# Optimization experiments

Hardware: AMD Instinct MI355X
Metric: run time of the kernel (lower is better)

Reference implementation:

```python
import jax, jax.numpy as jnp
import numpy as np

B, C, H, W = 2, 256, 64, 64
HEADS, SR = 8, 4
D = C // HEADS          # head dim = 32
N = H * W               # query length = 4096
EPS = 1e-5


def _conv(x, w, stride=1, pad=0, groups=1, b=None):
    out = jax.lax.conv_general_dilated(
        x, w, (stride, stride), [(pad, pad), (pad, pad)],
        dimension_numbers=('NCHW', 'OIHW', 'NCHW'),
        feature_group_count=groups)
    if b is not None:
        out = out + b[None, :, None, None]
    return out


def _bn(x, p):
    # p: [4, C] = (gamma, beta, running_mean, running_var), eval-mode BN
    g, b, m, v = p[0], p[1], p[2], p[3]
    s = g / jnp.sqrt(v + EPS)
    return (x - m[None, :, None, None]) * s[None, :, None, None] + b[None, :, None, None]


def setup_inputs() -> dict:
    key = jax.random.key(0)
    ks = iter(jax.random.split(key, 32))
    nrm = lambda shape, s=0.05: jax.random.normal(next(ks), shape, jnp.float32) * s
    def bnp():
        return jnp.stack([jnp.ones((C,), jnp.float32), jnp.zeros((C,), jnp.float32),
                          jax.random.normal(next(ks), (C,), jnp.float32) * 0.1,
                          jax.random.uniform(next(ks), (C,), jnp.float32) + 0.5])
    return dict(
        x=jax.random.normal(next(ks), (B, C, H, W), jnp.float32),
        relative_pos_enc=jax.random.normal(next(ks), (B, 2, 64, 64), jnp.float32),
        q_w=nrm((C, C, 1, 1)), q_b=jnp.zeros((C,), jnp.float32),
        kv_w=nrm((2 * C, C, 1, 1)), kv_b=jnp.zeros((2 * C,), jnp.float32),
        sr1_dw_w=nrm((C, 1, SR + 3, SR + 3)), sr1_bn1=bnp(),
        sr1_pw_w=nrm((C, 1, 1, 1), 0.5), sr1_bn2=bnp(),
        sr2_dw_w=nrm((C, 1, SR // 2 + 3, SR // 2 + 3)), sr2_bn1=bnp(),
        sr2_pw_w=nrm((C, 1, 1, 1), 0.5), sr2_bn2=bnp(),
        local_w=nrm((C, 1, 3, 3)), local_b=jnp.zeros((C,), jnp.float32),
    )


def reference(x, relative_pos_enc, q_w, q_b, kv_w, kv_b,
              sr1_dw_w, sr1_bn1, sr1_pw_w, sr1_bn2,
              sr2_dw_w, sr2_bn1, sr2_pw_w, sr2_bn2,
              local_w, local_b):
    scale = D ** -0.5
    # q: 1x1 conv -> [B, heads, N, D]; both branches use the FIRST half of heads
    q = _conv(x, q_w, b=q_b).reshape(B, HEADS, D, N).transpose(0, 1, 3, 2)
    qh = q[:, :HEADS // 2]

    def branch(dw_w, bn1, pw_w, bn2, stride, pad, rpe_slice):
        # SR path: depthwise conv + BN + ReLU, depthwise 1x1 + BN
        y = jax.nn.relu(_bn(_conv(x, dw_w, stride, pad, groups=C), bn1))
        y = _bn(_conv(y, pw_w, groups=C), bn2)
        # local 3x3 depthwise mixing with residual
        y = _conv(y, local_w, pad=1, groups=C, b=local_b) + y
        kv = _conv(y, kv_w, b=kv_b)                # [B, 2C, h', w']
        k, v = jnp.split(kv, 2, axis=1)
        L = 2 * y.shape[2] * y.shape[3]            # channel-fold doubles kv length
        k = k.reshape(B, HEADS // 2, D, L)
        v = v.reshape(B, HEADS // 2, D, L).transpose(0, 1, 3, 2)
        attn = jnp.einsum('bhnd,bhdl->bhnl', qh, k) * scale
        rpe = jax.image.resize(rpe_slice, (B, 1, N, L), method='bicubic')
        attn = jax.nn.softmax(attn + rpe, axis=-1)
        return jnp.einsum('bhnl,bhld->bhnd', attn, v)

    x1 = branch(sr1_dw_w, sr1_bn1, sr1_pw_w, sr1_bn2,
                SR, (SR + 3) // 2, relative_pos_enc[:, 0:1])
    x2 = branch(sr2_dw_w, sr2_bn1, sr2_pw_w, sr2_bn2,
                SR // 2, (SR // 2 + 3) // 2, relative_pos_enc[:, 1:2])
    out = jnp.concatenate([x1, x2], axis=-1)       # [B, heads//2, N, 2D]
    return out.reshape(B, C, H, W)
```

## Files before the change

### kernel.cpp

```cpp
#include <hip/hip_runtime.h>
#include <hip/hip_bf16.h>
#include <math.h>

#define NB 2
#define NC 256
#define HWIN 4096
#define NN 4096
#define ND 32
#define NHH 4
#define EPSV 1e-5f

typedef short short8 __attribute__((ext_vector_type(8)));
typedef float f32x4 __attribute__((ext_vector_type(4)));
typedef unsigned short u16;
typedef unsigned int u32;

#define OFF_T1   0
#define OFF_Y1   131072
#define OFF_T2   262144
#define OFF_Y2   786432
#define OFF_Q    1310720
#define OFF_KT1  1835008
#define OFF_VT1  1900544
#define OFF_KT2  1966080
#define OFF_VT2  2228224
#define OFF_RCT1 2490368
#define OFF_RCT2 2531328
#define OFF_WT   2695168
#define OFF_PO   2826240
#define OFF_PS   4923392
#define OFF_QWT  5054464

#define QSCALE 0.2550437314857726f
#define LOG2E  1.4426950408889634f

__device__ __forceinline__ u16 f2bf(float x) {
  unsigned u = __float_as_uint(x);
  u += 0x7fffu + ((u >> 16) & 1u);
  return (u16)(u >> 16);
}

__device__ __forceinline__ u32 pk_bf16(float a, float b) {
  __hip_bfloat162 h = __float22bfloat162_rn(make_float2(a, b));
  u32 r; __builtin_memcpy(&r, &h, 4);
  return r;
}

__device__ __forceinline__ float keysw(float t) {
  t = fabsf(t);
  float w;
  if (t < 1.f)       w = ((1.5f*t - 2.5f)*t)*t + 1.f;
  else if (t < 2.f)  w = ((-0.5f*t + 2.5f)*t - 4.f)*t + 2.f;
  else               w = 0.f;
  return w;
}

template<int KS, int STR, int PAD, int OH>
__device__ __forceinline__ void dwconv_body(int idx, const float* __restrict__ x,
    const float* __restrict__ dww, const float* __restrict__ bn1,
    const float* __restrict__ pww, const float* __restrict__ bn2,
    float* __restrict__ tout) {
  const int hw = OH*OH;
  int s = idx % hw; int c = (idx/hw) % NC; int b = idx/(hw*NC);
  int oy = s / OH, ox = s % OH;
  const float* xp = x + (b*NC + c)*HWIN;
  const float* wp = dww + c*KS*KS;
  float acc = 0.f;
  #pragma unroll
  for (int ky = 0; ky < KS; ++ky) {
    int iy = oy*STR - PAD + ky;
    if (iy < 0 || iy >= 64) continue;
    #pragma unroll
    for (int kx = 0; kx < KS; ++kx) {
      int ix = ox*STR - PAD + kx;
      if (ix < 0 || ix >= 64) continue;
      acc += xp[iy*64 + ix] * wp[ky*KS + kx];
    }
  }
  float s1 = bn1[c] * rsqrtf(bn1[3*NC + c] + EPSV);
  float z = (acc - bn1[2*NC + c])*s1 + bn1[NC + c];
  z = fmaxf(z, 0.f);
  float s2 = bn2[c] * rsqrtf(bn2[3*NC + c] + EPSV);
  z = z * (pww[c]*s2) + (bn2[NC + c] - bn2[2*NC + c]*s2);
  tout[idx] = z;
}

__device__ __forceinline__ void rpe_body(int idx, const float* __restrict__ rpe,
                                         u16* __restrict__ rcT, int L, int ch) {
  int r = idx & 63; int l = (idx >> 6) % L; int b = idx / (64*L);
  float f = ((float)l + 0.5f)*(64.f/(float)L) - 0.5f;
  int i0 = (int)floorf(f) - 1;
  const float* rp = rpe + ((b*2 + ch)*64 + r)*64;
  float v = 0.f, wsum = 0.f;
  #pragma unroll
  for (int j = 0; j < 4; ++j) {
    int i = i0 + j;
    if (i >= 0 && i < 64) {
      float w = keysw(f - (float)i);
      v += w * rp[i]; wsum += w;
    }
  }
  rcT[((size_t)(b*L + l))*80 + 4 + r] = f2bf(v / wsum);
}

__global__ void __launch_bounds__(256) prep_kernel(
    const float* __restrict__ x,
    const float* __restrict__ dw1, const float* __restrict__ bn11,
    const float* __restrict__ pw1, const float* __restrict__ bn12, float* __restrict__ t1,
    const float* __restrict__ dw2, const float* __restrict__ bn21,
    const float* __restrict__ pw2, const float* __restrict__ bn22, float* __restrict__ t2,
    const float* __restrict__ rpe, u16* __restrict__ rct1, u16* __restrict__ rct2,
    const float* __restrict__ kvw, float* __restrict__ wt,
    const float* __restrict__ qw, float* __restrict__ qwt) {
  int blk = blockIdx.x;
  int t = threadIdx.x;
  if (blk < 512) {
    dwconv_body<7,4,3,16>(blk*256 + t, x, dw1, bn11, pw1, bn12, t1);
  } else if (blk < 2560) {
    dwconv_body<5,2,2,32>((blk-512)*256 + t, x, dw2, bn21, pw2, bn22, t2);
  } else if (blk < 2816) {
    rpe_body((blk-2560)*256 + t, rpe, rct1, 512, 0);
  } else if (blk < 3840) {
    rpe_body((blk-2816)*256 + t, rpe, rct2, 2048, 1);
  } else if (blk < 3968) {
    int base = ((blk-3840)*256 + t)*4;
    float4 vv = *(const float4*)(kvw + base);
    int o = base >> 8, c = base & 255;
    wt[(c+0)*512 + o] = vv.x;
    wt[(c+1)*512 + o] = vv.y;
    wt[(c+2)*512 + o] = vv.z;
    wt[(c+3)*512 + o] = vv.w;
  } else {
    int base = ((blk-3968)*256 + t)*4;
    float4 vv = *(const float4*)(qw + base);
    int oc = base >> 8, c = base & 255;
    qwt[(c+0)*128 + oc] = vv.x;
    qwt[(c+1)*128 + oc] = vv.y;
    qwt[(c+2)*128 + oc] = vv.z;
    qwt[(c+3)*128 + oc] = vv.w;
  }
}

template<int OH>
__device__ __forceinline__ void local_body(int idx, const float* __restrict__ tin,
    const float* __restrict__ lw, const float* __restrict__ lb, float* __restrict__ yout) {
  const int hw = OH*OH;
  int s = idx % hw; int c = (idx/hw) % NC; int b = idx/(hw*NC);
  int oy = s/OH, ox = s%OH;
  const float* tp = tin + (b*NC + c)*hw;
  const float* wp = lw + c*9;
  float acc = lb[c];
  #pragma unroll
  for (int ky = 0; ky < 3; ++ky) {
    int iy = oy - 1 + ky;
    if (iy < 0 || iy >= OH) continue;
    #pragma unroll
    for (int kx = 0; kx < 3; ++kx) {
      int ix = ox - 1 + kx;
      if (ix < 0 || ix >= OH) continue;
      acc += tp[iy*OH + ix]*wp[ky*3 + kx];
    }
  }
  yout[idx] = acc + tp[s];
}

__global__ void __launch_bounds__(256) local_kernel(
    const float* __restrict__ t1, const float* __restrict__ t2,
    const float* __restrict__ lw, const float* __restrict__ lb,
    float* __restrict__ y1, float* __restrict__ y2) {
  int blk = blockIdx.x, t = threadIdx.x;
  if (blk < 512) local_body<16>(blk*256 + t, t1, lw, lb, y1);
  else           local_body<32>((blk-512)*256 + t, t2, lw, lb, y2);
}

__global__ void __launch_bounds__(256) kv_kernel(
    const float* __restrict__ y1, const float* __restrict__ y2,
    const float* __restrict__ wt, const float* __restrict__ kvb,
    u16* __restrict__ kt1, u16* __restrict__ vt1,
    u16* __restrict__ kt2, u16* __restrict__ vt2,
    const float* __restrict__ x, const float* __restrict__ qwt,
    const float* __restrict__ qb, u16* __restrict__ q) {
  __shared__ float sbuf[NC*16];
  int blk = blockIdx.x, t = threadIdx.x;
  if (blk < 640) {
    const float* y; u16 *kT, *vT; int hw, b, s0;
    if (blk < 128) { y = y1; kT = kt1; vT = vt1; hw = 256;  b = blk >> 6;  s0 = (blk & 63)*4; }
    else { int v = blk-128; y = y2; kT = kt2; vT = vt2; hw = 1024; b = v >> 8; s0 = (v & 255)*4; }
    #pragma unroll
    for (int j = 0; j < 4; ++j) {
      int idx = t + 256*j;
      int c = idx >> 2, i = idx & 3;
      sbuf[idx] = y[(b*NC + c)*hw + s0 + i];
    }
    __syncthreads();
    int L = 2*hw;
    for (int half = 0; half < 2; ++half) {
      int o = t + half*256;
      const float* wr = wt + o;
      float bias = kvb[o];
      float acc[4];
      #pragma unroll
      for (int i = 0; i < 4; ++i) acc[i] = bias;
      #pragma unroll 4
      for (int c = 0; c < NC; ++c) {
        float w = wr[c*512];
        #pragma unroll
        for (int i = 0; i < 4; ++i) acc[i] += w*sbuf[c*4 + i];
      }
      int oc = o & 255;
      int hh2 = oc >> 6, r = oc & 63, d = r >> 1, e = r & 1;
      if (half == 0) {
        u16* kp = kT + ((size_t)((b*NHH + hh2)*L + e*hw + s0))*ND + d;
        #pragma unroll
        for (int i = 0; i < 4; ++i) kp[i*ND] = f2bf(acc[i]);
      } else {
        u16* vp = vT + ((size_t)((b*NHH + hh2)*ND + d))*L + e*hw + s0;
        #pragma unroll
        for (int i = 0; i < 4; ++i) vp[i] = f2bf(acc[i]);
      }
    }
  } else {
    int blk2 = blk - 640;
    int b = blk2 >> 8;
    int n0 = (blk2 & 255) * 16;
    #pragma unroll
    for (int j = 0; j < 16; ++j) {
      int idx = t + 256*j;
      int c = idx >> 4, i = idx & 15;
      sbuf[idx] = x[(b*NC + c)*HWIN + n0 + i];
    }
    __syncthreads();
    int half = t >> 7, oc = t & 127;
    float bias = qb[oc];
    float acc[8];
    #pragma unroll
    for (int i = 0; i < 8; ++i) acc[i] = bias;
    #pragma unroll 4
    for (int c = 0; c < NC; ++c) {
      float w = qwt[c*128 + oc];
      #pragma unroll
      for (int i = 0; i < 8; ++i) acc[i] += w * sbuf[c*16 + half*8 + i];
    }
    int h = oc >> 5, d = oc & 31;
    u16* qp = q + (((size_t)(b*NHH + h))*NN + n0 + half*8)*ND + d;
    #pragma unroll
    for (int i = 0; i < 8; ++i) qp[i*ND] = f2bf(acc[i]*QSCALE);
  }
}

__global__ void __launch_bounds__(256) attn_kernel(
    const u16* __restrict__ qbf,
    const u16* __restrict__ kt1, const u16* __restrict__ vt1, const u16* __restrict__ rct1,
    const u16* __restrict__ kt2, const u16* __restrict__ vt2, const u16* __restrict__ rct2,
    u32* __restrict__ po32, float* __restrict__ ps,
    float* __restrict__ out) {
  __shared__ u16 kbuf[2][64*72];
  __shared__ u16 vbuf[2][32*72];
  __shared__ u32 pbuf_all[4][16*36];
  int u = blockIdx.x;
  int br, b, hh, rb, chunk;
  if (u < 512) { br = 0; b = u >> 8; hh = (u >> 6) & 3; rb = u & 63; chunk = 0; }
  else { int v = u - 512; br = 1; chunk = v & 3; rb = (v >> 2) & 63; hh = (v >> 8) & 3; b = v >> 10; }
  int L = br ? 2048 : 512;
  const u16* kT  = br ? kt2 : kt1;
  const u16* vT  = br ? vt2 : vt1;
  const u16* rcT = br ? rct2 : rct1;
  int l0base = chunk * 512;
  int tid = threadIdx.x;
  int w = tid >> 6, lane = tid & 63;
  int g = lane >> 4, lo = lane & 15;
  u32* pbuf = pbuf_all[w];
  u16* pbuf16 = (u16*)pbuf;
  int n = rb*64 + w*16 + lo;

  const u16* kbase = kT + (size_t)(b*NHH + hh)*L*ND;
  const u16* vbase = vT + (size_t)(b*NHH + hh)*ND*L;
  const u16* rcTb  = rcT + (size_t)b*L*80;

  short8 qf = *(const short8*)(qbf + (((size_t)(b*NHH + hh))*NN + n)*ND + 8*g);

  float fr = ((float)n + 0.5f)*(1.f/64.f) - 0.5f;
  int ri0 = (int)floorf(fr) - 1;
  int a = (w < 2) ? rb - 2 : rb - 1;
  int rmin = a & ~3;
  float wr4[4]; float wsum = 0.f;
  #pragma unroll
  for (int j = 0; j < 4; ++j) {
    int i = ri0 + j;
    float wv = (i >= 0 && i < 64) ? keysw(fr - (float)i) : 0.f;
    wr4[j] = wv; wsum += wv;
  }
  float invw = LOG2E / wsum;
  float wt8[8];
  #pragma unroll
  for (int s = 0; s < 8; ++s) {
    float acc = 0.f;
    #pragma unroll
    for (int j = 0; j < 4; ++j)
      acc += (ri0 + j - rmin == s) ? wr4[j]*invw : 0.f;
    wt8[s] = acc;
  }
  short8 wtf;
  {
    u32 p0 = pk_bf16(wt8[0], wt8[1]), p1 = pk_bf16(wt8[2], wt8[3]);
    u32 p2 = pk_bf16(wt8[4], wt8[5]), p3 = pk_bf16(wt8[6], wt8[7]);
    uint4 uu = make_uint4(p0, p1, p2, p3);
    wtf = __builtin_bit_cast(short8, uu);
    if (g != 0) wtf = (short8)0;
  }
  const u16* rcrow0 = rcTb + (rmin + 4);

  const f32x4 zero = {0.f, 0.f, 0.f, 0.f};
  float ssum = 0.f;
  f32x4 o0 = zero, o1 = zero;

  int kr_row = tid >> 2, kr_col = (tid & 3)*8;
  int vr_row = tid >> 3, vr_col = (tid & 7)*8;

  auto stageLoad = [&](short8& kr, short8& vr, int l0) {
    kr = *(const short8*)(kbase + (size_t)(l0 + kr_row)*ND + kr_col);
    vr = *(const short8*)(vbase + (size_t)vr_row*L + l0 + vr_col);
  };
  auto stageStore = [&](short8 kr, short8 vr, int buf) {
    *(short8*)(kbuf[buf] + kr_row*72 + kr_col) = kr;
    *(short8*)(vbuf[buf] + vr_row*72 + vr_col) = vr;
  };
  auto loadRC = [&](uint4 (&rc)[4], int l0) {
    #pragma unroll
    for (int c = 0; c < 4; ++c) {
      const u16* arow = rcrow0 + (size_t)(l0 + 16*c + lo)*80;
      uint2 ra = *(const uint2*)arow;
      uint2 rb2 = *(const uint2*)(arow + 4);
      rc[c] = make_uint4(ra.x, ra.y, rb2.x, rb2.y);
    }
  };

  short8 kr, vr;
  uint4 rcA[4], rcB[4];
  stageLoad(kr, vr, l0base);
  loadRC(rcA, l0base);
  stageStore(kr, vr, 0);
  __syncthreads();

  for (int t = 0; t < 8; ++t) {
    int buf = t & 1;
    if (t < 7) { stageLoad(kr, vr, l0base + (t+1)*64); loadRC(rcB, l0base + (t+1)*64); }
    const u16* lk = kbuf[buf];
    const u16* lv = vbuf[buf];
    f32x4 s4[4];
    #pragma unroll
    for (int c = 0; c < 4; ++c) {
      short8 rcf = __builtin_bit_cast(short8, rcA[c]);
      f32x4 accr = __builtin_amdgcn_mfma_f32_16x16x32_bf16(rcf, wtf, zero, 0, 0, 0);
      short8 kf = *(const short8*)(lk + (16*c + lo)*72 + 8*g);
      s4[c] = __builtin_amdgcn_mfma_f32_16x16x32_bf16(kf, qf, accr, 0, 0, 0);
    }
    float psum = 0.f;
    u32 pk[8];
    #pragma unroll
    for (int c = 0; c < 4; ++c) {
      float p0 = exp2f(s4[c][0]), p1 = exp2f(s4[c][1]);
      float p2 = exp2f(s4[c][2]), p3 = exp2f(s4[c][3]);
      psum += (p0 + p1) + (p2 + p3);
      pk[2*c]   = pk_bf16(p0, p1);
      pk[2*c+1] = pk_bf16(p2, p3);
    }
    ssum += psum;
    #pragma unroll
    for (int c = 0; c < 4; ++c)
      *(uint2*)(pbuf + lo*36 + 8*c + 2*g) = make_uint2(pk[2*c], pk[2*c+1]);
    short8 pf0 = *(const short8*)(pbuf16 + lo*72 + 8*g);
    short8 pf1 = *(const short8*)(pbuf16 + lo*72 + 32 + 8*g);
    short8 v00 = *(const short8*)(lv + lo*72 + 8*g);
    short8 v01 = *(const short8*)(lv + lo*72 + 32 + 8*g);
    short8 v10 = *(const short8*)(lv + (16+lo)*72 + 8*g);
    short8 v11 = *(const short8*)(lv + (16+lo)*72 + 32 + 8*g);
    o0 = __builtin_amdgcn_mfma_f32_16x16x32_bf16(v00, pf0, o0, 0, 0, 0);
    o1 = __builtin_amdgcn_mfma_f32_16x16x32_bf16(v10, pf0, o1, 0, 0, 0);
    o0 = __builtin_amdgcn_mfma_f32_16x16x32_bf16(v01, pf1, o0, 0, 0, 0);
    o1 = __builtin_amdgcn_mfma_f32_16x16x32_bf16(v11, pf1, o1, 0, 0, 0);
    if (t < 7) {
      stageStore(kr, vr, buf ^ 1);
      #pragma unroll
      for (int j = 0; j < 4; ++j) rcA[j] = rcB[j];
    }
    __syncthreads();
  }

  ssum += __shfl_xor(ssum, 16, 64);
  ssum += __shfl_xor(ssum, 32, 64);
  if (br == 0) {
    float inv = 1.f/ssum;
    f32x4 w0 = o0*inv, w1 = o1*inv;
    float* op = out + ((size_t)((b*NC + hh*64 + rb)*64 + (w*16 + lo)))*64;
    *(f32x4*)(op + 4*g)      = w0;
    *(f32x4*)(op + 16 + 4*g) = w1;
  } else {
    int bh = b*NHH + hh;
    int row = bh*NN + n;
    u32* pop = po32 + ((size_t)chunk*32768 + row)*16;
    pop[2*g]     = pk_bf16(o0[0], o0[1]);
    pop[2*g + 1] = pk_bf16(o0[2], o0[3]);
    pop[8 + 2*g]     = pk_bf16(o1[0], o1[1]);
    pop[8 + 2*g + 1] = pk_bf16(o1[2], o1[3]);
    if (g == 0) ps[(size_t)chunk*32768 + row] = ssum;
  }
}

__global__ void __launch_bounds__(256) combine_kernel(
    const u32* __restrict__ po32, const float* __restrict__ ps,
    float* __restrict__ out) {
  int gid = blockIdx.x*256 + threadIdx.x;
  int row = gid >> 2, part = gid & 3;
  float sden = ps[row] + ps[32768 + row] + ps[65536 + row] + ps[98304 + row];
  float inv = 1.f/sden;
  float o[8];
  #pragma unroll
  for (int i = 0; i < 8; ++i) o[i] = 0.f;
  #pragma unroll
  for (int chunk = 0; chunk < 4; ++chunk) {
    const u32* pp = po32 + ((size_t)chunk*32768 + row)*16 + part*4;
    uint4 a = *(const uint4*)pp;
    u32 av[4] = {a.x, a.y, a.z, a.w};
    #pragma unroll
    for (int j = 0; j < 4; ++j) {
      o[2*j]   += __uint_as_float(av[j] << 16);
      o[2*j+1] += __uint_as_float(av[j] & 0xffff0000u);
    }
  }
  int bh = row >> 12, n = row & 4095;
  float* op = out + ((size_t)(((bh>>2)*NC + (bh&3)*64 + (n>>6))*64 + (n&63)))*64 + 32 + part*8;
  #pragma unroll
  for (int j = 0; j < 2; ++j) {
    f32x4 v = {o[4*j]*inv, o[4*j+1]*inv, o[4*j+2]*inv, o[4*j+3]*inv};
    *(f32x4*)(op + 4*j) = v;
  }
}

extern "C" void kernel_launch(void* const* d_in, const int* in_sizes, int n_in,
                              void* d_out, int out_size, void* d_ws, size_t ws_size,
                              hipStream_t stream) {
  const float* x    = (const float*)d_in[0];
  const float* rpe  = (const float*)d_in[1];
  const float* qw   = (const float*)d_in[2];
  const float* qb   = (const float*)d_in[3];
  const float* kvw  = (const float*)d_in[4];
  const float* kvb  = (const float*)d_in[5];
  const float* dw1  = (const float*)d_in[6];
  const float* bn11 = (const float*)d_in[7];
  const float* pw1  = (const float*)d_in[8];
  const float* bn12 = (const float*)d_in[9];
  const float* dw2  = (const float*)d_in[10];
  const float* bn21 = (const float*)d_in[11];
  const float* pw2  = (const float*)d_in[12];
  const float* bn22 = (const float*)d_in[13];
  const float* lw   = (const float*)d_in[14];
  const float* lb   = (const float*)d_in[15];
  float* out = (float*)d_out;
  float* ws  = (float*)d_ws;

  float* t1   = ws + OFF_T1;
  float* y1   = ws + OFF_Y1;
  float* t2   = ws + OFF_T2;
  float* y2   = ws + OFF_Y2;
  u16*   q    = (u16*)(ws + OFF_Q);
  u16*   kt1  = (u16*)(ws + OFF_KT1);
  u16*   vt1  = (u16*)(ws + OFF_VT1);
  u16*   kt2  = (u16*)(ws + OFF_KT2);
  u16*   vt2  = (u16*)(ws + OFF_VT2);
  u16*   rct1 = (u16*)(ws + OFF_RCT1);
  u16*   rct2 = (u16*)(ws + OFF_RCT2);
  float* wt   = ws + OFF_WT;
  u32*   po32 = (u32*)(ws + OFF_PO);
  float* ps   = ws + OFF_PS;
  float* qwt  = ws + OFF_QWT;

  hipLaunchKernelGGL(prep_kernel, dim3(4000), dim3(256), 0, stream,
                     x, dw1, bn11, pw1, bn12, t1, dw2, bn21, pw2, bn22, t2,
                     rpe, rct1, rct2, kvw, wt, qw, qwt);
  hipLaunchKernelGGL(local_kernel, dim3(2560), dim3(256), 0, stream,
                     t1, t2, lw, lb, y1, y2);
  hipLaunchKernelGGL(kv_kernel, dim3(1152), dim3(256), 0, stream,
                     y1, y2, wt, kvb, kt1, vt1, kt2, vt2, x, qwt, qb, q);
  hipLaunchKernelGGL(attn_kernel, dim3(2560), dim3(256), 0, stream,
                     q, kt1, vt1, rct1, kt2, vt2, rct2, po32, ps, out);
  hipLaunchKernelGGL(combine_kernel, dim3(512), dim3(256), 0, stream,
                     po32, ps, out);
}
```

Baseline: 195.6 us.

## Fuse local depthwise conv into KV projection kernel and widen spatial tile

Merges the 3x3 depthwise local mixing into the KV projection kernel, so y1/y2 are computed directly into shared memory rather than written to and re-read from global memory. This removes one kernel launch. Each KV block now handles 8 spatial positions instead of 4 and computes both K and V outputs per thread, so every weight load feeds more FMAs. The cost is fewer blocks (320 instead of 640 for KV) and recomputation of neighbor reads from global memory inside each block.

```diff
diff --git a/kernel.cpp b/kernel.cpp
--- a/kernel.cpp
+++ b/kernel.cpp
@@ -16,9 +16,7 @@
 typedef unsigned int u32;
 
 #define OFF_T1   0
-#define OFF_Y1   131072
 #define OFF_T2   262144
-#define OFF_Y2   786432
 #define OFF_Q    1310720
 #define OFF_KT1  1835008
 #define OFF_VT1  1900544
@@ -141,96 +139,80 @@
   }
 }
 
-template<int OH>
-__device__ __forceinline__ void local_body(int idx, const float* __restrict__ tin,
-    const float* __restrict__ lw, const float* __restrict__ lb, float* __restrict__ yout) {
-  const int hw = OH*OH;
-  int s = idx % hw; int c = (idx/hw) % NC; int b = idx/(hw*NC);
-  int oy = s/OH, ox = s%OH;
-  const float* tp = tin + (b*NC + c)*hw;
-  const float* wp = lw + c*9;
-  float acc = lb[c];
-  #pragma unroll
-  for (int ky = 0; ky < 3; ++ky) {
-    int iy = oy - 1 + ky;
-    if (iy < 0 || iy >= OH) continue;
-    #pragma unroll
-    for (int kx = 0; kx < 3; ++kx) {
-      int ix = ox - 1 + kx;
-      if (ix < 0 || ix >= OH) continue;
-      acc += tp[iy*OH + ix]*wp[ky*3 + kx];
-    }
-  }
-  yout[idx] = acc + tp[s];
-}
-
-__global__ void __launch_bounds__(256) local_kernel(
-    const float* __restrict__ t1, const float* __restrict__ t2,
+__global__ void __launch_bounds__(256) localkv_kernel(
+    const float* __restrict__ t1in, const float* __restrict__ t2in,
     const float* __restrict__ lw, const float* __restrict__ lb,
-    float* __restrict__ y1, float* __restrict__ y2) {
-  int blk = blockIdx.x, t = threadIdx.x;
-  if (blk < 512) local_body<16>(blk*256 + t, t1, lw, lb, y1);
-  else           local_body<32>((blk-512)*256 + t, t2, lw, lb, y2);
-}
-
-__global__ void __launch_bounds__(256) kv_kernel(
-    const float* __restrict__ y1, const float* __restrict__ y2,
     const float* __restrict__ wt, const float* __restrict__ kvb,
     u16* __restrict__ kt1, u16* __restrict__ vt1,
     u16* __restrict__ kt2, u16* __restrict__ vt2,
     const float* __restrict__ x, const float* __restrict__ qwt,
     const float* __restrict__ qb, u16* __restrict__ q) {
   __shared__ float sbuf[NC*16];
-  int blk = blockIdx.x, t = threadIdx.x;
-  if (blk < 640) {
-    const float* y; u16 *kT, *vT; int hw, b, s0;
-    if (blk < 128) { y = y1; kT = kt1; vT = vt1; hw = 256;  b = blk >> 6;  s0 = (blk & 63)*4; }
-    else { int v = blk-128; y = y2; kT = kt2; vT = vt2; hw = 1024; b = v >> 8; s0 = (v & 255)*4; }
-    #pragma unroll
-    for (int j = 0; j < 4; ++j) {
-      int idx = t + 256*j;
-      int c = idx >> 2, i = idx & 3;
-      sbuf[idx] = y[(b*NC + c)*hw + s0 + i];
+  int blk = blockIdx.x, tid = threadIdx.x;
+  if (blk < 320) {
+    const float* tin; u16 *kT, *vT; int OH, hw, b, s0;
+    if (blk < 64) { tin = t1in; kT = kt1; vT = vt1; OH = 16; hw = 256;  b = blk >> 5;  s0 = (blk & 31)*8; }
+    else { int v = blk-64; tin = t2in; kT = kt2; vT = vt2; OH = 32; hw = 1024; b = v >> 7; s0 = (v & 127)*8; }
+    int oy = s0 / OH, ox0 = s0 % OH;
+    int ci = tid >> 3, i = tid & 7;
+    int ox = ox0 + i;
+    #pragma unroll
+    for (int p = 0; p < 8; ++p) {
+      int c = p*32 + ci;
+      const float* tp = tin + (b*NC + c)*hw;
+      const float* wp = lw + c*9;
+      float acc = lb[c];
+      #pragma unroll
+      for (int dy = 0; dy < 3; ++dy) {
+        int iy = oy + dy - 1;
+        if (iy < 0 || iy >= OH) continue;
+        #pragma unroll
+        for (int dx = 0; dx < 3; ++dx) {
+          int ix = ox + dx - 1;
+          if (ix < 0 || ix >= OH) continue;
+          acc += tp[iy*OH + ix]*wp[dy*3 + dx];
+        }
+      }
+      acc += tp[oy*OH + ox];
+      sbuf[c*12 + i] = acc;
     }
     __syncthreads();
+    float acc0[8], acc1[8];
+    float b0 = kvb[tid], b1 = kvb[tid + 256];
+    #pragma unroll
+    for (int j = 0; j < 8; ++j) { acc0[j] = b0; acc1[j] = b1; }
+    #pragma unroll 4
+    for (int c = 0; c < NC; ++c) {
+      f32x4 ya = *(const f32x4*)(sbuf + c*12);
+      f32x4 yb = *(const f32x4*)(sbuf + c*12 + 4);
+      float w0 = wt[c*512 + tid];
+      float w1 = wt[c*512 + tid + 256];
+      #pragma unroll
+      for (int j = 0; j < 4; ++j) {
+        acc0[j]   += w0*ya[j];  acc0[4+j] += w0*yb[j];
+        acc1[j]   += w1*ya[j];  acc1[4+j] += w1*yb[j];
+      }
+    }
+    int hh2 = tid >> 6, r = tid & 63, d = r >> 1, e = r & 1;
     int L = 2*hw;
-    for (int half = 0; half < 2; ++half) {
-      int o = t + half*256;
-      const float* wr = wt + o;
-      float bias = kvb[o];
-      float acc[4];
-      #pragma unroll
-      for (int i = 0; i < 4; ++i) acc[i] = bias;
-      #pragma unroll 4
-      for (int c = 0; c < NC; ++c) {
-        float w = wr[c*512];
-        #pragma unroll
-        for (int i = 0; i < 4; ++i) acc[i] += w*sbuf[c*4 + i];
-      }
-      int oc = o & 255;
-      int hh2 = oc >> 6, r = oc & 63, d = r >> 1, e = r & 1;
-      if (half == 0) {
-        u16* kp = kT + ((size_t)((b*NHH + hh2)*L + e*hw + s0))*ND + d;
-        #pragma unroll
-        for (int i = 0; i < 4; ++i) kp[i*ND] = f2bf(acc[i]);
-      } else {
-        u16* vp = vT + ((size_t)((b*NHH + hh2)*ND + d))*L + e*hw + s0;
-        #pragma unroll
-        for (int i = 0; i < 4; ++i) vp[i] = f2bf(acc[i]);
-      }
-    }
+    u16* kp = kT + ((size_t)((b*NHH + hh2)*L + e*hw + s0))*ND + d;
+    #pragma unroll
+    for (int j = 0; j < 8; ++j) kp[j*ND] = f2bf(acc0[j]);
+    u16* vp = vT + ((size_t)((b*NHH + hh2)*ND + d))*L + e*hw + s0;
+    #pragma unroll
+    for (int j = 0; j < 8; ++j) vp[j] = f2bf(acc1[j]);
   } else {
-    int blk2 = blk - 640;
+    int blk2 = blk - 320;
     int b = blk2 >> 8;
     int n0 = (blk2 & 255) * 16;
     #pragma unroll
     for (int j = 0; j < 16; ++j) {
-      int idx = t + 256*j;
+      int idx = tid + 256*j;
       int c = idx >> 4, i = idx & 15;
       sbuf[idx] = x[(b*NC + c)*HWIN + n0 + i];
     }
     __syncthreads();
-    int half = t >> 7, oc = t & 127;
+    int half = tid >> 7, oc = tid & 127;
     float bias = qb[oc];
     float acc[8];
     #pragma unroll
@@ -460,9 +442,7 @@
   float* ws  = (float*)d_ws;
 
   float* t1   = ws + OFF_T1;
-  float* y1   = ws + OFF_Y1;
   float* t2   = ws + OFF_T2;
-  float* y2   = ws + OFF_Y2;
   u16*   q    = (u16*)(ws + OFF_Q);
   u16*   kt1  = (u16*)(ws + OFF_KT1);
   u16*   vt1  = (u16*)(ws + OFF_VT1);
@@ -478,10 +458,8 @@
   hipLaunchKernelGGL(prep_kernel, dim3(4000), dim3(256), 0, stream,
                      x, dw1, bn11, pw1, bn12, t1, dw2, bn21, pw2, bn22, t2,
                      rpe, rct1, rct2, kvw, wt, qw, qwt);
-  hipLaunchKernelGGL(local_kernel, dim3(2560), dim3(256), 0, stream,
-                     t1, t2, lw, lb, y1, y2);
-  hipLaunchKernelGGL(kv_kernel, dim3(1152), dim3(256), 0, stream,
-                     y1, y2, wt, kvb, kt1, vt1, kt2, vt2, x, qwt, qb, q);
+  hipLaunchKernelGGL(localkv_kernel, dim3(832), dim3(256), 0, stream,
+                     t1, t2, lw, lb, wt, kvb, kt1, vt1, kt2, vt2, x, qwt, qb, q);
   hipLaunchKernelGGL(attn_kernel, dim3(2560), dim3(256), 0, stream,
                      q, kt1, vt1, rct1, kt2, vt2, rct2, po32, ps, out);
   hipLaunchKernelGGL(combine_kernel, dim3(512), dim3(256), 0, stream,
```

New measurement: 190.5 us. 1.03x faster.
